# Performance work log

Hardware: AMD Instinct MI355X
Metric: run time of the kernel (lower is better)

The kernel has to match this reference:

```python
import jax, jax.numpy as jnp
import numpy as np

B, H, L = 16, 512, 2048
N2 = 32  # d_state/2 complex modes
DT_MIN, DT_MAX = 1e-3, 1e-1


def setup_inputs() -> dict:
    key = jax.random.key(0)
    ks = jax.random.split(key, 8)
    u = jax.random.normal(ks[0], (B, H, L), dtype=jnp.float32)
    D = jax.random.normal(ks[1], (H,), dtype=jnp.float32)
    # log-uniform timescales in [DT_MIN, DT_MAX]
    r = jax.random.uniform(ks[2], (H,), dtype=jnp.float32)
    log_dt = (np.log(DT_MIN) + r * (np.log(DT_MAX) - np.log(DT_MIN))).astype(jnp.float32)
    C_re = jax.random.normal(ks[3], (H, N2), dtype=jnp.float32)
    C_im = jax.random.normal(ks[4], (H, N2), dtype=jnp.float32)
    W1 = jax.random.normal(ks[5], (L, 2 * H), dtype=jnp.float32) / np.float32(np.sqrt(L))
    b1 = jnp.zeros((2 * H,), dtype=jnp.float32)
    W2 = jax.random.normal(ks[6], (2 * H, H), dtype=jnp.float32) / np.float32(np.sqrt(2 * H))
    b2 = jnp.zeros((H,), dtype=jnp.float32)
    return {"u": u, "D": D, "log_dt": log_dt, "C_re": C_re, "C_im": C_im,
            "W1": W1, "b1": b1, "W2": W2, "b2": b2}


def _s4d_kernel(log_dt, C_re, C_im, length):
    # S4D-Lin: A_n = -1/2 + i*pi*n
    n = jnp.arange(N2, dtype=jnp.float32)
    A = -0.5 + 1j * jnp.pi * n                      # (N2,)
    dt = jnp.exp(log_dt)                             # (H,)
    dtA = dt[:, None] * A[None, :]                   # (H, N2)
    C = (C_re + 1j * C_im) * (jnp.exp(dtA) - 1.0) / A
    # Vandermonde: k[h, l] = 2 * Re sum_n C[h,n] * exp(dtA[h,n] * l)
    K = jnp.exp(dtA[:, :, None] * jnp.arange(length, dtype=jnp.float32))  # (H, N2, L)
    return 2.0 * jnp.einsum('hn,hnl->hl', C, K).real  # (H, L)


def reference(u, D, log_dt, C_re, C_im, W1, b1, W2, b2):
    # u: (B, H, L)
    k = _s4d_kernel(log_dt, C_re, C_im, L)           # (H, L)
    k_f = jnp.fft.rfft(k, n=2 * L, axis=-1)          # (H, L+1)
    u_f = jnp.fft.rfft(u, n=2 * L, axis=-1)          # (B, H, L+1)
    y = jnp.fft.irfft(u_f * k_f[None], n=2 * L, axis=-1)[..., :L]
    y = y + u * D[:, None]
    y = jax.nn.gelu(y, approximate=False)
    # keras Conv1D(k=1) / tanh / Dense applied to channels-first tensor:
    # dense over last axis L -> 2H, tanh, dense 2H -> H
    y = jnp.tanh(jnp.einsum('bhl,lf->bhf', y, W1) + b1)  # (B, H, 2H)
    y = jnp.einsum('bhf,fo->bho', y, W2) + b2            # (B, H, H)
    return y
```

## Files before the change

### kernel.cpp

```cpp
#include <hip/hip_runtime.h>
#include <math.h>

#define B_  16
#define H_  512
#define L_  2048
#define N2_ 32
#define NC_ 16
#define LC_ 128

typedef __attribute__((ext_vector_type(8))) short short8;
typedef __attribute__((ext_vector_type(4))) float f32x4;

__device__ __forceinline__ short f2bf(float x) {
    unsigned u = __builtin_bit_cast(unsigned, x);
    u += 0x7fffu + ((u >> 16) & 1u);
    return (short)(u >> 16);
}
__device__ __forceinline__ float bf2f(unsigned short s) {
    unsigned u = ((unsigned)s) << 16;
    return __builtin_bit_cast(float, u);
}

__global__ void k0_table(const float* __restrict__ log_dt,
                         const float* __restrict__ C_re,
                         const float* __restrict__ C_im,
                         float4* __restrict__ tab) {
    int idx = blockIdx.x * blockDim.x + threadIdx.x;
    if (idx >= H_ * N2_) return;
    int h = idx >> 5, n = idx & 31;
    float dt = expf(log_dt[h]);
    float e  = expf(-0.5f * dt);
    float th = 3.14159265358979323846f * (float)n * dt;
    float lr = e * cosf(th), li = e * sinf(th);
    float ar = -0.5f, ai = 3.14159265358979323846f * (float)n;
    float den = ar * ar + ai * ai;
    float x = lr - 1.0f, y = li;
    float nr = (x * ar + y * ai) / den;
    float ni = (y * ar - x * ai) / den;
    float cr = C_re[idx], ci = C_im[idx];
    tab[idx] = make_float4(lr, li, cr * nr - ci * ni, cr * ni + ci * nr);
}

__global__ void t0_pow(const float4* __restrict__ tab, float2* __restrict__ POW) {
    int t = blockIdx.x * 256 + threadIdx.x;
    if (t >= H_ * N2_) return;
    int h = t >> 5;
    float4 v = tab[t];
    float lr = v.x, li = v.y;
    float pr = 1.0f, pi = 0.0f;
    float2* base = POW + (size_t)h * 129 * N2_ + (t & 31);
    for (int m = 0; m <= 128; ++m) {
        base[(size_t)m * N2_] = make_float2(pr, pi);
        float npr = pr * lr - pi * li;
        float npi = pr * li + pi * lr;
        pr = npr; pi = npi;
    }
}

__global__ void t_ktab(const float4* __restrict__ tab, const float2* __restrict__ POW,
                       const float* __restrict__ Dv, float* __restrict__ ktab) {
    int t = blockIdx.x * 256 + threadIdx.x;
    if (t >= H_ * 128) return;
    int h = t >> 7, m = t & 127;
    const float2* P = POW + (size_t)h * 129 * N2_ + (size_t)m * N2_;
    const float4* tb = tab + h * N2_;
    float s = 0.0f;
    for (int n = 0; n < N2_; ++n) {
        float2 p = P[n];
        float4 v = tb[n];
        s += v.z * p.x - v.w * p.y;
    }
    ktab[t] = 2.0f * s + (m == 0 ? Dv[h] : 0.0f);
}

__global__ void __launch_bounds__(256)
t1_fill(const float4* __restrict__ tab, const float2* __restrict__ POW,
        const float* __restrict__ ktab, short* __restrict__ Psw,
        short* __restrict__ Vsw) {
    int t = blockIdx.x * 256 + threadIdx.x;
    int sub = t & 7;
    int rowg = t >> 3;
    int h = rowg / 320, row = rowg % 320;
    if (row < 192) {
        short8 s0, s1;
        if (row < 128) {
            int l = row;
#pragma unroll
            for (int mm = 0; mm < 8; ++mm) {
                int m0 = sub * 16 + mm, m1 = m0 + 8;
                s0[mm] = (m0 <= l) ? f2bf(ktab[h * 128 + (l - m0)]) : (short)0;
                s1[mm] = (m1 <= l) ? f2bf(ktab[h * 128 + (l - m1)]) : (short)0;
            }
        } else {
            int j = row - 128, nn = j >> 1, part = j & 1;
            const float2* P = POW + (size_t)h * 129 * N2_ + nn;
#pragma unroll
            for (int mm = 0; mm < 8; ++mm) {
                int m0 = sub * 16 + mm, m1 = m0 + 8;
                float2 p0 = P[(size_t)(127 - m0) * N2_];
                float2 p1 = P[(size_t)(127 - m1) * N2_];
                s0[mm] = f2bf(part ? p0.y : p0.x);
                s1[mm] = f2bf(part ? p1.y : p1.x);
            }
        }
        *(short8*)(Psw + ((size_t)(h * 16 + sub * 2 + 0) * 192 + row) * 8) = s0;
        *(short8*)(Psw + ((size_t)(h * 16 + sub * 2 + 1) * 192 + row) * 8) = s1;
    } else {
        int l = row - 192;
        const float2* P = POW + (size_t)h * 129 * N2_ + (size_t)(l + 1) * N2_;
        const float4* tb = tab + h * N2_;
        short8 s;
#pragma unroll
        for (int jj = 0; jj < 8; ++jj) {
            int j = sub * 8 + jj, nn = j >> 1;
            float2 p = P[nn];
            float4 cv = tb[nn];
            float re = cv.z * p.x - cv.w * p.y;
            float im = cv.z * p.y + cv.w * p.x;
            s[jj] = f2bf((j & 1) ? -2.0f * im : 2.0f * re);
        }
        *(short8*)(Vsw + ((size_t)(h * 8 + sub) * 128 + l) * 8) = s;
    }
}

__global__ void __launch_bounds__(512)
conv_mfma(const float* __restrict__ u, const short* __restrict__ Psw,
          float* __restrict__ E, short* __restrict__ Ybuf) {
    __shared__ char smem[65536];
    short* Ps = (short*)smem;
    short* As = (short*)(smem + 49152);
    short* Ys = (short*)smem;
    int h = blockIdx.x;
    int tid = threadIdx.x;
    {
        const short8* Pg = (const short8*)(Psw + (size_t)h * 24576);
        short8* PsV = (short8*)Ps;
#pragma unroll
        for (int j = 0; j < 6; ++j) PsV[tid + j * 512] = Pg[tid + j * 512];
    }
    int row = tid >> 1, half = tid & 1;
    int b0 = row >> 4, c0 = row & 15;
    const float* up = u + ((size_t)(b0 * H_ + h)) * L_ + (size_t)c0 * LC_ + half * 16;
    short8* AsV = (short8*)As;

    int lane = tid & 63, wave = tid >> 6;
    int wm = wave >> 1, wn = wave & 1;
    int lrow = lane & 15, lk = lane >> 4;
    const short8* AsF = (const short8*)As;
    const short8* PsF = (const short8*)Ps;

    f32x4 acc[4][6] = {};
    float4 fv0 = *(const float4*)(up + 0);
    float4 fv1 = *(const float4*)(up + 4);
    float4 fv2 = *(const float4*)(up + 8);
    float4 fv3 = *(const float4*)(up + 12);
    for (int ks = 0; ks < 4; ++ks) {
        __syncthreads();
        short8 s0, s1;
        s0[0] = f2bf(fv0.x); s0[1] = f2bf(fv0.y); s0[2] = f2bf(fv0.z); s0[3] = f2bf(fv0.w);
        s0[4] = f2bf(fv1.x); s0[5] = f2bf(fv1.y); s0[6] = f2bf(fv1.z); s0[7] = f2bf(fv1.w);
        s1[0] = f2bf(fv2.x); s1[1] = f2bf(fv2.y); s1[2] = f2bf(fv2.z); s1[3] = f2bf(fv2.w);
        s1[4] = f2bf(fv3.x); s1[5] = f2bf(fv3.y); s1[6] = f2bf(fv3.z); s1[7] = f2bf(fv3.w);
        AsV[(half * 2 + 0) * 256 + row] = s0;
        AsV[(half * 2 + 1) * 256 + row] = s1;
        __syncthreads();
        if (ks < 3) {
            const float* nx = up + (ks + 1) * 32;
            fv0 = *(const float4*)(nx + 0);
            fv1 = *(const float4*)(nx + 4);
            fv2 = *(const float4*)(nx + 8);
            fv3 = *(const float4*)(nx + 12);
        }
        short8 af[4], bfr[6];
#pragma unroll
        for (int m = 0; m < 4; ++m)
            af[m] = AsF[lk * 256 + wm * 64 + m * 16 + lrow];
#pragma unroll
        for (int n = 0; n < 6; ++n)
            bfr[n] = PsF[(ks * 4 + lk) * 192 + wn * 96 + n * 16 + lrow];
#pragma unroll
        for (int m = 0; m < 4; ++m)
#pragma unroll
            for (int n = 0; n < 6; ++n)
                acc[m][n] = __builtin_amdgcn_mfma_f32_16x16x32_bf16(
                    af[m], bfr[n], acc[m][n], 0, 0, 0);
    }
    __syncthreads();

#pragma unroll
    for (int nf = 0; nf < 6; ++nf) {
        int col = wn * 96 + nf * 16 + lrow;
#pragma unroll
        for (int mf = 0; mf < 4; ++mf) {
            int rb = wm * 64 + mf * 16 + lk * 4;
#pragma unroll
            for (int r = 0; r < 4; ++r) {
                int Rr = rb + r;
                float vv = acc[mf][nf][r];
                if (col < 128) {
                    Ys[Rr * 128 + col] = f2bf(vv);
                } else {
                    int bb = Rr >> 4, cc = Rr & 15;
                    E[((size_t)(bb * H_ + h) * NC_ + cc) * 64 + (col - 128)] = vv;
                }
            }
        }
    }
    __syncthreads();

    const short8* YsV = (const short8*)Ys;
#pragma unroll
    for (int it = 0; it < 8; ++it) {
        int sidx = it * 512 + tid;
        int rr = sidx >> 4;
        int colq = sidx & 15;
        int bb = rr >> 4, cc = rr & 15;
        *(short8*)(Ybuf + ((size_t)(bb * H_ + h)) * L_ + (size_t)cc * LC_ + colq * 8)
            = YsV[sidx];
    }
}

__global__ void k2_scan(const float* __restrict__ log_dt, float2* __restrict__ ES) {
    int t = blockIdx.x * 256 + threadIdx.x;
    if (t >= B_ * H_ * N2_) return;
    int n  = t & 31;
    int h  = (t >> 5) & (H_ - 1);
    int bh = t >> 5;
    float dt = expf(log_dt[h]);
    float e  = expf(-0.5f * dt * (float)LC_);
    float th = 3.14159265358979323846f * (float)n * dt * (float)LC_;
    float Lr = e * cosf(th), Li = e * sinf(th);
    float cr = 0.0f, ci = 0.0f;
    float2* base = ES + (size_t)bh * NC_ * N2_ + n;
#pragma unroll
    for (int c = 0; c < NC_; ++c) {
        float2 Ev = base[(size_t)c * N2_];
        base[(size_t)c * N2_] = make_float2(cr, ci);
        float ncr = fmaf(Lr, cr, fmaf(-Li, ci, Ev.x));
        float nci = fmaf(Lr, ci, fmaf(Li, cr, Ev.y));
        cr = ncr; ci = nci;
    }
}

__global__ void __launch_bounds__(256)
dcarry_mfma(const float* __restrict__ ES, const short* __restrict__ Vsw,
            const short* __restrict__ Ybuf, short* __restrict__ gbf) {
    __shared__ char smem[32768];
    short* Sa = (short*)smem;
    short* Vb = (short*)(smem + 16384);
    short* Ys = (short*)smem;
    int h = blockIdx.x, mh = blockIdx.y;
    int tid = threadIdx.x;
    {
        const short8* Vg = (const short8*)(Vsw + (size_t)h * 8192);
        short8* VbV = (short8*)Vb;
#pragma unroll
        for (int j = 0; j < 4; ++j) VbV[tid + j * 256] = Vg[tid + j * 256];
    }
    int row = tid >> 1, half = tid & 1;
    int R = mh * 128 + row, b = R >> 4, c = R & 15;
    {
        const float* sp = ES + ((size_t)(b * H_ + h) * NC_ + c) * 64 + half * 32;
        short8* SaV = (short8*)Sa;
#pragma unroll
        for (int gg = 0; gg < 4; ++gg) {
            float4 f0 = *(const float4*)(sp + gg * 8);
            float4 f1 = *(const float4*)(sp + gg * 8 + 4);
            short8 s;
            s[0] = f2bf(f0.x); s[1] = f2bf(f0.y); s[2] = f2bf(f0.z); s[3] = f2bf(f0.w);
            s[4] = f2bf(f1.x); s[5] = f2bf(f1.y); s[6] = f2bf(f1.z); s[7] = f2bf(f1.w);
            SaV[(half * 4 + gg) * 128 + row] = s;
        }
    }
    __syncthreads();
    int lane = tid & 63, wave = tid >> 6;
    int wm = wave >> 1, wn = wave & 1;
    int lrow = lane & 15, lk = lane >> 4;
    const short8* SaF = (const short8*)Sa;
    const short8* VbF = (const short8*)Vb;
    f32x4 acc[4][4] = {};
#pragma unroll
    for (int ks = 0; ks < 2; ++ks) {
        int g = ks * 4 + lk;
        short8 af[4], bf[4];
#pragma unroll
        for (int m = 0; m < 4; ++m)
            af[m] = SaF[g * 128 + wm * 64 + m * 16 + lrow];
#pragma unroll
        for (int n = 0; n < 4; ++n)
            bf[n] = VbF[g * 128 + wn * 64 + n * 16 + lrow];
#pragma unroll
        for (int m = 0; m < 4; ++m)
#pragma unroll
            for (int n = 0; n < 4; ++n)
                acc[m][n] = __builtin_amdgcn_mfma_f32_16x16x32_bf16(
                    af[m], bf[n], acc[m][n], 0, 0, 0);
    }
    __syncthreads();

#pragma unroll
    for (int nf = 0; nf < 4; ++nf) {
        int l = wn * 64 + nf * 16 + lrow;
#pragma unroll
        for (int mf = 0; mf < 4; ++mf) {
            int rb = wm * 64 + mf * 16 + lk * 4;
#pragma unroll
            for (int r = 0; r < 4; ++r)
                Ys[(rb + r) * 128 + l] = f2bf(acc[mf][nf][r]);
        }
    }
    __syncthreads();

    const short8* YsV = (const short8*)Ys;
#pragma unroll
    for (int it = 0; it < 8; ++it) {
        int sidx = it * 256 + tid;
        int rr = sidx >> 4;
        int colq = sidx & 15;
        int Rr = mh * 128 + rr, bb = Rr >> 4, cc = Rr & 15;
        size_t gaddr = ((size_t)(bb * H_ + h)) * L_ + (size_t)cc * LC_ + colq * 8;
        short8 yv = *(const short8*)(Ybuf + gaddr);
        short8 cv = YsV[sidx];
        short8 o;
#pragma unroll
        for (int j = 0; j < 8; ++j) {
            float y = bf2f((unsigned short)yv[j]) + bf2f((unsigned short)cv[j]);
            o[j] = f2bf(0.5f * y * (1.0f + erff(y * 0.70710678118654752f)));
        }
        *(short8*)(gbf + gaddr) = o;
    }
}

__global__ void __launch_bounds__(256)
wtrans(const float* __restrict__ W, short* __restrict__ Wt, int K, int N) {
    __shared__ short tile[32][33];
    int bk = blockIdx.x * 32, bn = blockIdx.y * 32;
    int tx = threadIdx.x & 31, ty = threadIdx.x >> 5;
#pragma unroll
    for (int i = 0; i < 4; ++i)
        tile[ty + i * 8][tx] = f2bf(W[(size_t)(bk + ty + i * 8) * N + bn + tx]);
    __syncthreads();
#pragma unroll
    for (int i = 0; i < 4; ++i)
        Wt[(size_t)(bn + ty + i * 8) * K + bk + tx] = tile[tx][ty + i * 8];
}

template<bool TANH, bool OUTBF>
__global__ void __launch_bounds__(512)
gemm_mfma(const short* __restrict__ A, const short* __restrict__ Bt,
          const float* __restrict__ bias, void* __restrict__ Cout,
          int M, int N, int K) {
    __shared__ short As[2][128 * 36];
    __shared__ short Bs[2][128 * 36];
    int tid  = threadIdx.x;
    int lane = tid & 63;
    int wave = tid >> 6;
    int wm = wave >> 2, wn = wave & 3;
    int lrow = lane & 15, kblk = lane >> 4;
    int row0 = blockIdx.x * 128, col0 = blockIdx.y * 128;

    int srow = tid >> 2;
    int sk   = (tid & 3) * 8;
    const short* Ag = A  + (size_t)(row0 + srow) * K + sk;
    const short* Bg = Bt + (size_t)(col0 + srow) * K + sk;
    int si = srow * 36 + sk;

    f32x4 acc[4][2] = {};
    const int NT = K >> 5;

    short8 pa = *(const short8*)(Ag),      pb = *(const short8*)(Bg);
    *(short8*)&As[0][si] = pa;
    *(short8*)&Bs[0][si] = pb;
    short8 qa = *(const short8*)(Ag + 32), qb = *(const short8*)(Bg + 32);
    __syncthreads();

    for (int t = 0; t < NT; t += 2) {
        if (t + 2 < NT) {
            int ko = (t + 2) << 5;
            pa = *(const short8*)(Ag + ko);
            pb = *(const short8*)(Bg + ko);
        }
        {
            short8 af[4], bf[2];
#pragma unroll
            for (int m = 0; m < 4; ++m)
                af[m] = *(const short8*)&As[0][(wm * 64 + m * 16 + lrow) * 36 + kblk * 8];
#pragma unroll
            for (int n = 0; n < 2; ++n)
                bf[n] = *(const short8*)&Bs[0][(wn * 32 + n * 16 + lrow) * 36 + kblk * 8];
#pragma unroll
            for (int m = 0; m < 4; ++m)
#pragma unroll
                for (int n = 0; n < 2; ++n)
                    acc[m][n] = __builtin_amdgcn_mfma_f32_16x16x32_bf16(
                        af[m], bf[n], acc[m][n], 0, 0, 0);
        }
        *(short8*)&As[1][si] = qa;
        *(short8*)&Bs[1][si] = qb;
        __syncthreads();

        if (t + 3 < NT) {
            int ko = (t + 3) << 5;
            qa = *(const short8*)(Ag + ko);
            qb = *(const short8*)(Bg + ko);
        }
        {
            short8 af[4], bf[2];
#pragma unroll
            for (int m = 0; m < 4; ++m)
                af[m] = *(const short8*)&As[1][(wm * 64 + m * 16 + lrow) * 36 + kblk * 8];
#pragma unroll
            for (int n = 0; n < 2; ++n)
                bf[n] = *(const short8*)&Bs[1][(wn * 32 + n * 16 + lrow) * 36 + kblk * 8];
#pragma unroll
            for (int m = 0; m < 4; ++m)
#pragma unroll
                for (int n = 0; n < 2; ++n)
                    acc[m][n] = __builtin_amdgcn_mfma_f32_16x16x32_bf16(
                        af[m], bf[n], acc[m][n], 0, 0, 0);
        }
        if (t + 2 < NT) {
            *(short8*)&As[0][si] = pa;
            *(short8*)&Bs[0][si] = pb;
        }
        __syncthreads();
    }

#pragma unroll
    for (int n = 0; n < 2; ++n) {
        int col = col0 + wn * 32 + n * 16 + lrow;
        float bb = bias[col];
#pragma unroll
        for (int m = 0; m < 4; ++m) {
            int rowb = row0 + wm * 64 + m * 16 + kblk * 4;
#pragma unroll
            for (int r = 0; r < 4; ++r) {
                float v = acc[m][n][r] + bb;
                if (TANH) v = tanhf(v);
                if (OUTBF) ((short*)Cout)[(size_t)(rowb + r) * N + col] = f2bf(v);
                else       ((float*)Cout)[(size_t)(rowb + r) * N + col] = v;
            }
        }
    }
}

extern "C" void kernel_launch(void* const* d_in, const int* in_sizes, int n_in,
                              void* d_out, int out_size, void* d_ws, size_t ws_size,
                              hipStream_t stream) {
    const float* u     = (const float*)d_in[0];
    const float* D     = (const float*)d_in[1];
    const float* logdt = (const float*)d_in[2];
    const float* C_re  = (const float*)d_in[3];
    const float* C_im  = (const float*)d_in[4];
    const float* W1    = (const float*)d_in[5];
    const float* b1    = (const float*)d_in[6];
    const float* W2    = (const float*)d_in[7];
    const float* b2    = (const float*)d_in[8];
    float* out = (float*)d_out;

    char* p = (char*)d_ws;
    float4* tab = (float4*)p;            p += 262144;
    char* regionA = p;                   p += 33554432;
    float2* POW  = (float2*)regionA;
    float*  ktab = (float*)(regionA + 16908288);
    short*  Ybuf = (short*)regionA;
    short* Psw = (short*)p;              p += 25165824;
    short* Vsw = (short*)p;              p += 8388608;
    float* E   = (float*)p;              p += 33554432;
    short* gbf = (short*)p;              p += 33554432;
    short* tb  = (short*)p;              p += 16777216;
    short* w1t = (short*)p;              p += 4194304;
    short* w2t = (short*)p;

    k0_table<<<H_ * N2_ / 256, 256, 0, stream>>>(logdt, C_re, C_im, tab);
    t0_pow  <<<H_ * N2_ / 256, 256, 0, stream>>>(tab, POW);
    t_ktab  <<<H_ * 128 / 256, 256, 0, stream>>>(tab, POW, D, ktab);
    t1_fill <<<H_ * 320 * 8 / 256, 256, 0, stream>>>(tab, POW, ktab, Psw, Vsw);
    wtrans  <<<dim3(L_ / 32, 2 * H_ / 32), 256, 0, stream>>>(W1, w1t, L_, 2 * H_);
    wtrans  <<<dim3(2 * H_ / 32, H_ / 32), 256, 0, stream>>>(W2, w2t, 2 * H_, H_);

    conv_mfma  <<<H_, 512, 0, stream>>>(u, Psw, E, Ybuf);
    k2_scan    <<<B_ * H_ * N2_ / 256, 256, 0, stream>>>(logdt, (float2*)E);
    dcarry_mfma<<<dim3(H_, 2), 256, 0, stream>>>(E, Vsw, Ybuf, gbf);

    gemm_mfma<true, true ><<<dim3(B_ * H_ / 128, 2 * H_ / 128), 512, 0, stream>>>(
        gbf, w1t, b1, tb, B_ * H_, 2 * H_, L_);
    gemm_mfma<false, false><<<dim3(B_ * H_ / 128, H_ / 128), 512, 0, stream>>>(
        tb, w2t, b2, out, B_ * H_, H_, 2 * H_);
}
```

Measured before the change: 190.8 us.

## Use direct global-to-LDS loads and 64x64 wave tiles in bf16 GEMM

Rewrites the MFMA GEMM so operand tiles are copied straight from global memory into LDS with global_load_lds, skipping the register staging step. The LDS layout becomes k-block-major with no padding. The block shrinks to 4 waves, each computing a 64x64 sub-tile (4x4 MFMAs) for more reuse per fragment load. The double-buffered loop now advances one k-tile per iteration. This trades occupancy and possible LDS bank conflicts for lower load-instruction overhead and higher arithmetic intensity per wave.

```diff
diff --git a/kernel.cpp b/kernel.cpp
--- a/kernel.cpp
+++ b/kernel.cpp
@@ -19,6 +19,12 @@
 __device__ __forceinline__ float bf2f(unsigned short s) {
     unsigned u = ((unsigned)s) << 16;
     return __builtin_bit_cast(float, u);
+}
+
+__device__ __forceinline__ void gl16(const short* g, short* l) {
+    __builtin_amdgcn_global_load_lds(
+        (__attribute__((address_space(1))) const void*)g,
+        (__attribute__((address_space(3))) void*)l, 16, 0, 0);
 }
 
 __global__ void k0_table(const float* __restrict__ log_dt,
@@ -346,93 +352,69 @@
 }
 
 template<bool TANH, bool OUTBF>
-__global__ void __launch_bounds__(512)
+__global__ void __launch_bounds__(256)
 gemm_mfma(const short* __restrict__ A, const short* __restrict__ Bt,
           const float* __restrict__ bias, void* __restrict__ Cout,
           int M, int N, int K) {
-    __shared__ short As[2][128 * 36];
-    __shared__ short Bs[2][128 * 36];
+    __shared__ short As[2][4 * 128 * 8];
+    __shared__ short Bs[2][4 * 128 * 8];
     int tid  = threadIdx.x;
     int lane = tid & 63;
     int wave = tid >> 6;
-    int wm = wave >> 2, wn = wave & 3;
-    int lrow = lane & 15, kblk = lane >> 4;
+    int wm = wave >> 1, wn = wave & 1;
+    int lrow = lane & 15, lk = lane >> 4;
     int row0 = blockIdx.x * 128, col0 = blockIdx.y * 128;
 
-    int srow = tid >> 2;
-    int sk   = (tid & 3) * 8;
-    const short* Ag = A  + (size_t)(row0 + srow) * K + sk;
-    const short* Bg = Bt + (size_t)(col0 + srow) * K + sk;
-    int si = srow * 36 + sk;
-
-    f32x4 acc[4][2] = {};
+    int sr = tid & 127, kb = tid >> 7;
+    const short* Ag0 = A  + (size_t)(row0 + sr) * K + kb * 8;
+    const short* Ag1 = A  + (size_t)(row0 + sr) * K + (kb + 2) * 8;
+    const short* Bg0 = Bt + (size_t)(col0 + sr) * K + kb * 8;
+    const short* Bg1 = Bt + (size_t)(col0 + sr) * K + (kb + 2) * 8;
+    int so0 = (kb * 128 + sr) * 8;
+    int so1 = ((kb + 2) * 128 + sr) * 8;
+
+    f32x4 acc[4][4] = {};
     const int NT = K >> 5;
 
-    short8 pa = *(const short8*)(Ag),      pb = *(const short8*)(Bg);
-    *(short8*)&As[0][si] = pa;
-    *(short8*)&Bs[0][si] = pb;
-    short8 qa = *(const short8*)(Ag + 32), qb = *(const short8*)(Bg + 32);
-    __syncthreads();
-
-    for (int t = 0; t < NT; t += 2) {
-        if (t + 2 < NT) {
-            int ko = (t + 2) << 5;
-            pa = *(const short8*)(Ag + ko);
-            pb = *(const short8*)(Bg + ko);
-        }
-        {
-            short8 af[4], bf[2];
-#pragma unroll
-            for (int m = 0; m < 4; ++m)
-                af[m] = *(const short8*)&As[0][(wm * 64 + m * 16 + lrow) * 36 + kblk * 8];
-#pragma unroll
-            for (int n = 0; n < 2; ++n)
-                bf[n] = *(const short8*)&Bs[0][(wn * 32 + n * 16 + lrow) * 36 + kblk * 8];
-#pragma unroll
-            for (int m = 0; m < 4; ++m)
-#pragma unroll
-                for (int n = 0; n < 2; ++n)
-                    acc[m][n] = __builtin_amdgcn_mfma_f32_16x16x32_bf16(
-                        af[m], bf[n], acc[m][n], 0, 0, 0);
-        }
-        *(short8*)&As[1][si] = qa;
-        *(short8*)&Bs[1][si] = qb;
+    gl16(Ag0, &As[0][so0]);
+    gl16(Ag1, &As[0][so1]);
+    gl16(Bg0, &Bs[0][so0]);
+    gl16(Bg1, &Bs[0][so1]);
+    __syncthreads();
+
+    int cur = 0;
+    for (int t = 0; t < NT; ++t) {
+        if (t + 1 < NT) {
+            int ko = (t + 1) << 5;
+            gl16(Ag0 + ko, &As[cur ^ 1][so0]);
+            gl16(Ag1 + ko, &As[cur ^ 1][so1]);
+            gl16(Bg0 + ko, &Bs[cur ^ 1][so0]);
+            gl16(Bg1 + ko, &Bs[cur ^ 1][so1]);
+        }
+        short8 af[4], bf[4];
+#pragma unroll
+        for (int m = 0; m < 4; ++m)
+            af[m] = *(const short8*)&As[cur][(lk * 128 + wm * 64 + m * 16 + lrow) * 8];
+#pragma unroll
+        for (int n = 0; n < 4; ++n)
+            bf[n] = *(const short8*)&Bs[cur][(lk * 128 + wn * 64 + n * 16 + lrow) * 8];
+#pragma unroll
+        for (int m = 0; m < 4; ++m)
+#pragma unroll
+            for (int n = 0; n < 4; ++n)
+                acc[m][n] = __builtin_amdgcn_mfma_f32_16x16x32_bf16(
+                    af[m], bf[n], acc[m][n], 0, 0, 0);
         __syncthreads();
-
-        if (t + 3 < NT) {
-            int ko = (t + 3) << 5;
-            qa = *(const short8*)(Ag + ko);
-            qb = *(const short8*)(Bg + ko);
-        }
-        {
-            short8 af[4], bf[2];
-#pragma unroll
-            for (int m = 0; m < 4; ++m)
-                af[m] = *(const short8*)&As[1][(wm * 64 + m * 16 + lrow) * 36 + kblk * 8];
-#pragma unroll
-            for (int n = 0; n < 2; ++n)
-                bf[n] = *(const short8*)&Bs[1][(wn * 32 + n * 16 + lrow) * 36 + kblk * 8];
-#pragma unroll
-            for (int m = 0; m < 4; ++m)
-#pragma unroll
-                for (int n = 0; n < 2; ++n)
-                    acc[m][n] = __builtin_amdgcn_mfma_f32_16x16x32_bf16(
-                        af[m], bf[n], acc[m][n], 0, 0, 0);
-        }
-        if (t + 2 < NT) {
-            *(short8*)&As[0][si] = pa;
-            *(short8*)&Bs[0][si] = pb;
-        }
-        __syncthreads();
-    }
-
-#pragma unroll
-    for (int n = 0; n < 2; ++n) {
-        int col = col0 + wn * 32 + n * 16 + lrow;
+        cur ^= 1;
+    }
+
+#pragma unroll
+    for (int n = 0; n < 4; ++n) {
+        int col = col0 + wn * 64 + n * 16 + lrow;
         float bb = bias[col];
 #pragma unroll
         for (int m = 0; m < 4; ++m) {
-            int rowb = row0 + wm * 64 + m * 16 + kblk * 4;
+            int rowb = row0 + wm * 64 + m * 16 + lk * 4;
 #pragma unroll
             for (int r = 0; r < 4; ++r) {
                 float v = acc[m][n][r] + bb;
@@ -483,8 +465,8 @@
     k2_scan    <<<B_ * H_ * N2_ / 256, 256, 0, stream>>>(logdt, (float2*)E);
     dcarry_mfma<<<dim3(H_, 2), 256, 0, stream>>>(E, Vsw, Ybuf, gbf);
 
-    gemm_mfma<true, true ><<<dim3(B_ * H_ / 128, 2 * H_ / 128), 512, 0, stream>>>(
+    gemm_mfma<true, true ><<<dim3(B_ * H_ / 128, 2 * H_ / 128), 256, 0, stream>>>(
         gbf, w1t, b1, tb, B_ * H_, 2 * H_, L_);
-    gemm_mfma<false, false><<<dim3(B_ * H_ / 128, H_ / 128), 512, 0, stream>>>(
+    gemm_mfma<false, false><<<dim3(B_ * H_ / 128, H_ / 128), 256, 0, stream>>>(
         tb, w2t, b2, out, B_ * H_, H_, 2 * H_);
 }
```

Measured after the change: 256.3 us. 1.34x slower.

## Use 256x128 block tile with register prefetch for first GEMM

Applied to the files above, without the earlier changes.

Adds a new GEMM kernel for the large L->2H projection. Each block computes a 256x128 output tile, with each wave owning a 64x64 sub-tile (4x4 MFMA accumulators), so each loaded fragment feeds more MFMA work. Global loads for the next K slices are prefetched into registers two steps ahead, while shared memory drops from double buffering to a single buffer. The aim is higher arithmetic intensity and less LDS and global traffic per FLOP, at the cost of more registers, lower occupancy and half as many blocks (256 instead of 512).

```diff
diff --git a/kernel.cpp b/kernel.cpp
--- a/kernel.cpp
+++ b/kernel.cpp
@@ -347,6 +347,85 @@
 
 template<bool TANH, bool OUTBF>
 __global__ void __launch_bounds__(512)
+gemm_mfma_w(const short* __restrict__ A, const short* __restrict__ Bt,
+            const float* __restrict__ bias, void* __restrict__ Cout,
+            int M, int N, int K) {
+    __shared__ short As[256 * 36 + 8];
+    __shared__ short Bs[128 * 36 + 8];
+    int tid  = threadIdx.x;
+    int lane = tid & 63;
+    int wave = tid >> 6;
+    int wm = wave >> 1, wn = wave & 1;
+    int lrow = lane & 15, lk = lane >> 4;
+    int row0 = blockIdx.x * 256, col0 = blockIdx.y * 128;
+
+    int arow = tid >> 1, ak = (tid & 1) * 16;
+    const short* AgP = A + (size_t)(row0 + arow) * K + ak;
+    int saA = arow * 36 + ak;
+    int brow = tid >> 2, bk = (tid & 3) * 8;
+    const short* BgP = Bt + (size_t)(col0 + brow) * K + bk;
+    int saB = brow * 36 + bk;
+
+    f32x4 acc[4][4] = {};
+    const int NT = K >> 5;
+
+    short8 xa0 = *(const short8*)(AgP),      xa1 = *(const short8*)(AgP + 8);
+    short8 xb  = *(const short8*)(BgP);
+    short8 ya0 = *(const short8*)(AgP + 32), ya1 = *(const short8*)(AgP + 40);
+    short8 yb  = *(const short8*)(BgP + 32);
+
+    auto gstep = [&](short8& A0, short8& A1, short8& Bv, int tnext) {
+        __syncthreads();
+        *(short8*)&As[saA]     = A0;
+        *(short8*)&As[saA + 8] = A1;
+        *(short8*)&Bs[saB]     = Bv;
+        __syncthreads();
+        if (tnext < NT) {
+            int ko = tnext << 5;
+            A0 = *(const short8*)(AgP + ko);
+            A1 = *(const short8*)(AgP + ko + 8);
+            Bv = *(const short8*)(BgP + ko);
+        }
+        short8 af[4], bf[4];
+#pragma unroll
+        for (int m = 0; m < 4; ++m)
+            af[m] = *(const short8*)&As[(wm * 64 + m * 16 + lrow) * 36 + lk * 8];
+#pragma unroll
+        for (int n = 0; n < 4; ++n)
+            bf[n] = *(const short8*)&Bs[(wn * 64 + n * 16 + lrow) * 36 + lk * 8];
+#pragma unroll
+        for (int m = 0; m < 4; ++m)
+#pragma unroll
+            for (int n = 0; n < 4; ++n)
+                acc[m][n] = __builtin_amdgcn_mfma_f32_16x16x32_bf16(
+                    af[m], bf[n], acc[m][n], 0, 0, 0);
+    };
+
+    for (int t = 0; t < NT; t += 2) {
+        gstep(xa0, xa1, xb, t + 2);
+        gstep(ya0, ya1, yb, t + 3);
+    }
+
+#pragma unroll
+    for (int n = 0; n < 4; ++n) {
+        int col = col0 + wn * 64 + n * 16 + lrow;
+        float bb = bias[col];
+#pragma unroll
+        for (int m = 0; m < 4; ++m) {
+            int rowb = row0 + wm * 64 + m * 16 + lk * 4;
+#pragma unroll
+            for (int r = 0; r < 4; ++r) {
+                float v = acc[m][n][r] + bb;
+                if (TANH) v = tanhf(v);
+                if (OUTBF) ((short*)Cout)[(size_t)(rowb + r) * N + col] = f2bf(v);
+                else       ((float*)Cout)[(size_t)(rowb + r) * N + col] = v;
+            }
+        }
+    }
+}
+
+template<bool TANH, bool OUTBF>
+__global__ void __launch_bounds__(512)
 gemm_mfma(const short* __restrict__ A, const short* __restrict__ Bt,
           const float* __restrict__ bias, void* __restrict__ Cout,
           int M, int N, int K) {
@@ -483,7 +562,7 @@
     k2_scan    <<<B_ * H_ * N2_ / 256, 256, 0, stream>>>(logdt, (float2*)E);
     dcarry_mfma<<<dim3(H_, 2), 256, 0, stream>>>(E, Vsw, Ybuf, gbf);
 
-    gemm_mfma<true, true ><<<dim3(B_ * H_ / 128, 2 * H_ / 128), 512, 0, stream>>>(
+    gemm_mfma_w<true, true ><<<dim3(B_ * H_ / 256, 2 * H_ / 128), 512, 0, stream>>>(
         gbf, w1t, b1, tb, B_ * H_, 2 * H_, L_);
     gemm_mfma<false, false><<<dim3(B_ * H_ / 128, H_ / 128), 512, 0, stream>>>(
         tb, w2t, b2, out, B_ * H_, H_, 2 * H_);
```

Result: slower. 206.6 us (+8.3%).
